# Performance work log

Hardware: AMD Instinct MI355X
Metric: run time of the kernel (lower is better)

## Reference

```python
import jax, jax.numpy as jnp
import numpy as np

B, S, E, H, L = 64, 256, 640, 512, 2  # batch, seq_len, input_size(=embed+sum_depth), rnn_size, num_layers
ZDIM = L * 2 * 2 * H  # ziphidden output dim = num_layers * num_dirs * (h|c) * H = 4096


def setup_inputs() -> dict:
    key = jax.random.key(0)
    ks = jax.random.split(key, 16)
    s = 0.05  # small init scale (~1/sqrt(H)) to avoid gate saturation
    f32 = jnp.float32
    inp = {
        "input": jax.random.normal(ks[0], (B, S, E), f32),
        "eps": jax.random.normal(ks[1], (B, ZDIM), f32),
        # layer 0 (input E), stacked over 2 directions [fwd, rev]
        "w_ih0": jax.random.normal(ks[2], (2, 4 * H, E), f32) * s,
        "w_hh0": jax.random.normal(ks[3], (2, 4 * H, H), f32) * s,
        "b_ih0": jax.random.normal(ks[4], (2, 4 * H), f32) * s,
        "b_hh0": jax.random.normal(ks[5], (2, 4 * H), f32) * s,
        # layer 1 (input 2H from bidirectional layer-0 output)
        "w_ih1": jax.random.normal(ks[6], (2, 4 * H, 2 * H), f32) * s,
        "w_hh1": jax.random.normal(ks[7], (2, 4 * H, H), f32) * s,
        "b_ih1": jax.random.normal(ks[8], (2, 4 * H), f32) * s,
        "b_hh1": jax.random.normal(ks[9], (2, 4 * H), f32) * s,
        # linear heads (layer_dim*2 -> layer_dim*2)
        "W_mu": jax.random.normal(ks[10], (ZDIM, ZDIM), f32) * 0.02,
        "b_mu": jax.random.normal(ks[11], (ZDIM,), f32) * 0.02,
        "W_var": jax.random.normal(ks[12], (ZDIM, ZDIM), f32) * 0.02,
        "b_var": jax.random.normal(ks[13], (ZDIM,), f32) * 0.02,
    }
    return inp


def _lstm_cell(x, h, c, wih, whh, b):
    # gates order i, f, g, o (PyTorch convention)
    g = x @ wih.T + h @ whh.T + b
    i, f, gg, o = jnp.split(g, 4, axis=-1)
    c2 = jax.nn.sigmoid(f) * c + jax.nn.sigmoid(i) * jnp.tanh(gg)
    h2 = jax.nn.sigmoid(o) * jnp.tanh(c2)
    return h2, c2


def reference(input, eps, w_ih0, w_hh0, b_ih0, b_hh0, w_ih1, w_hh1, b_ih1, b_hh1, W_mu, b_mu, W_var, b_var):
    # Module does input.view(seq_len, batch, embed) (a reshape, not transpose) then
    # steps the LSTM one timestep at a time for seq_len-1 steps. Since each call is
    # a length-1 sequence, both directions see the same single step independently.
    x_seq = input.reshape(S, B, E)[: S - 1]
    W_ih, W_hh = [w_ih0, w_ih1], [w_hh0, w_hh1]
    Bias = [b_ih0 + b_hh0, b_ih1 + b_hh1]

    h0 = jnp.zeros((2 * L, B, H), input.dtype)  # [l0f, l0r, l1f, l1r]
    c0 = jnp.zeros((2 * L, B, H), input.dtype)

    def step(carry, x):
        h, c = carry
        hs, cs = [], []
        inp_l = x
        for l in range(L):
            hf, cf = _lstm_cell(inp_l, h[2 * l], c[2 * l], W_ih[l][0], W_hh[l][0], Bias[l][0])
            hr, cr = _lstm_cell(inp_l, h[2 * l + 1], c[2 * l + 1], W_ih[l][1], W_hh[l][1], Bias[l][1])
            hs += [hf, hr]
            cs += [cf, cr]
            inp_l = jnp.concatenate([hf, hr], axis=-1)  # layer output feeds next layer
        return (jnp.stack(hs), jnp.stack(cs)), None

    (hF, cF), _ = jax.lax.scan(step, (h0, c0), x_seq)

    # ziphidden: cat(h, c, dim=2) -> transpose(0,1) -> view(B, -1)
    z = jnp.concatenate([hF, cF], axis=2)            # [2L, B, 2H]
    z = jnp.transpose(z, (1, 0, 2)).reshape(B, -1)   # [B, ZDIM]

    mu = z @ W_mu.T + b_mu
    logvar = z @ W_var.T + b_var
    # reparameterize (training mode) with externally supplied eps
    return mu + eps * jnp.exp(0.5 * logvar)
```

## Files before the change

kernel.cpp:

```cpp
#include <hip/hip_runtime.h>
#include <hip/hip_bf16.h>
#include <cstddef>
#include <cstdint>

#define B     64
#define S     256
#define E     640
#define H     512
#define TSTEPS (S - 1)
#define ZDIM  4096
#define KT    64
#define HS    (B * H)
#define CELL64 8192

typedef __attribute__((ext_vector_type(8)))  __bf16 bf16x8;
typedef __attribute__((ext_vector_type(16))) float  f32x16;
typedef unsigned long long ull;

__device__ __forceinline__ float sigf(float x) { return 1.0f / (1.0f + __expf(-x)); }
__device__ __forceinline__ float tanhfast(float x) { return 1.0f - 2.0f / (__expf(2.0f * x) + 1.0f); }

__device__ __forceinline__ unsigned short f2bf(float f) {
    union { float f; unsigned u; } x; x.f = f;
    unsigned r = x.u + 0x7fffu + ((x.u >> 16) & 1u);
    return (unsigned short)(r >> 16);
}
__device__ __forceinline__ float bf2f(unsigned short u) {
    union { unsigned u; float f; } x; x.u = ((unsigned)u) << 16;
    return x.f;
}
__device__ __forceinline__ unsigned pk2(float a, float b) {
    return (unsigned)f2bf(a) | ((unsigned)f2bf(b) << 16);
}

#define HSTORE64(p, v) __hip_atomic_store((p), (v), __ATOMIC_RELAXED, __HIP_MEMORY_SCOPE_AGENT)
#define HSTORE32(p, v) __hip_atomic_store((p), (v), __ATOMIC_RELAXED, __HIP_MEMORY_SCOPE_AGENT)
#define HLOAD32(p)     __hip_atomic_load((p), __ATOMIC_RELAXED, __HIP_MEMORY_SCOPE_AGENT)

__device__ __forceinline__ uint4 cld16(const void* p) {
    uint4 v;
    asm volatile("global_load_dwordx4 %0, %1, off sc0 sc1"
                 : "=v"(v) : "v"(p) : "memory");
    return v;
}
__device__ __forceinline__ void cwait0() {
    asm volatile("s_waitcnt vmcnt(0)" ::: "memory");
    __builtin_amdgcn_sched_barrier(0);
}
__device__ __forceinline__ bf16x8 u2b(uint4 u) {
    union { uint4 u; bf16x8 b; } x; x.u = u; return x.b;
}


__global__ __launch_bounds__(256) void conv_x_kernel(
    const float* __restrict__ in, unsigned short* __restrict__ out, int n8)
{
    int i = blockIdx.x * 256 + threadIdx.x;
    if (i >= n8) return;
    const float4* p = (const float4*)(in + (size_t)i * 8);
    float4 a = p[0], b = p[1];
    unsigned short* o = out + (size_t)i * 8;
    o[0] = f2bf(a.x); o[1] = f2bf(a.y); o[2] = f2bf(a.z); o[3] = f2bf(a.w);
    o[4] = f2bf(b.x); o[5] = f2bf(b.y); o[6] = f2bf(b.z); o[7] = f2bf(b.w);
}

__global__ __launch_bounds__(256) void repack_w_kernel(
    const float* __restrict__ in, unsigned short* __restrict__ out, int K)
{
    int kc = K / 8;
    int i = blockIdx.x * 256 + threadIdx.x;
    if (i >= 2 * 2048 * kc) return;
    int k8 = i % kc;
    int n  = (i / kc) & 2047;
    int d  = i / (kc * 2048);
    int srow = (n & 3) * 512 + (n >> 2);
    const float* src = in + ((size_t)d * 2048 + srow) * K + (size_t)k8 * 8;
    unsigned short* dst = out + ((size_t)d * 2048 + n) * K + (size_t)k8 * 8;
    #pragma unroll
    for (int q = 0; q < 8; ++q) dst[q] = f2bf(src[q]);
}

__global__ __launch_bounds__(256) void pack_bias_kernel(
    const float* __restrict__ bih, const float* __restrict__ bhh, float* __restrict__ out)
{
    int i = blockIdx.x * 256 + threadIdx.x;
    if (i >= 4096) return;
    int d = i >> 11, n = i & 2047;
    int s = d * 2048 + (n & 3) * 512 + (n >> 2);
    out[i] = bih[s] + bhh[s];
}

__global__ __launch_bounds__(256) void xproj_kernel(
    const unsigned short* __restrict__ xb,
    const unsigned short* __restrict__ w0p,
    unsigned short* __restrict__ xp)
{
    extern __shared__ __align__(16) char lds[];
    const int tid = threadIdx.x;
    const int l   = tid & 63;
    const int w   = tid >> 6;
    const int wm  = w & 1, wn = w >> 1;
    const int d   = blockIdx.x >> 5;
    const int n0  = (blockIdx.x & 31) * 64;

    for (int idx = tid; idx < 64 * 80; idx += 256) {
        int r = idx / 80, k8 = idx % 80;
        bf16x8 v = *(const bf16x8*)(w0p + ((size_t)d*2048 + n0 + r)*640 + (size_t)k8*8);
        int o = k8*16 + r*16; o -= (o >= 1280) ? 1280 : 0;
        *(bf16x8*)(lds + r*1280 + o) = v;
    }
    __syncthreads();

    const int lrow  = wn * 32 + (l & 31);
    const int khalf = l >> 5;
    const char* ldsrow = lds + (size_t)lrow * 1280;
    const int rot = lrow * 16 + khalf * 16;
    const int t0 = blockIdx.y * 64;
    const int t1 = (t0 + 64 < TSTEPS) ? (t0 + 64) : TSTEPS;

    for (int t = t0; t < t1; ++t) {
        f32x16 a0, a1;
#pragma unroll
        for (int r = 0; r < 16; ++r) { a0[r] = 0.f; a1[r] = 0.f; }
        const unsigned short* Ax = xb + ((size_t)t*B + wm*32 + (l & 31))*E + khalf*8;
#pragma unroll 8
        for (int k0 = 0; k0 < E; k0 += 16) {
            bf16x8 a = *(const bf16x8*)(Ax + k0);
            int o = k0*2 + rot; o -= (o >= 1280) ? 1280 : 0;
            bf16x8 b = *(const bf16x8*)(ldsrow + o);
            if ((k0 >> 4) & 1) a1 = __builtin_amdgcn_mfma_f32_32x32x16_bf16(a, b, a1, 0, 0, 0);
            else               a0 = __builtin_amdgcn_mfma_f32_32x32x16_bf16(a, b, a0, 0, 0, 0);
        }
        size_t base = ((((size_t)t*2 + d)*64 + (n0 >> 5) + wn)*2 + wm)*1024 + (size_t)l*16;
        unsigned short* dst = xp + base;
        uint4 o0, o1;
        o0.x = pk2(a0[0]+a1[0],  a0[1]+a1[1]);
        o0.y = pk2(a0[2]+a1[2],  a0[3]+a1[3]);
        o0.z = pk2(a0[4]+a1[4],  a0[5]+a1[5]);
        o0.w = pk2(a0[6]+a1[6],  a0[7]+a1[7]);
        o1.x = pk2(a0[8]+a1[8],  a0[9]+a1[9]);
        o1.y = pk2(a0[10]+a1[10], a0[11]+a1[11]);
        o1.z = pk2(a0[12]+a1[12], a0[13]+a1[13]);
        o1.w = pk2(a0[14]+a1[14], a0[15]+a1[15]);
        *(uint4*)dst       = o0;
        *(uint4*)(dst + 8) = o1;
    }
}

__device__ __forceinline__ void poll1(const unsigned* flags, int cell,
                                      unsigned tgt, int l)
{
    const unsigned* p0 = flags + (size_t)(cell*128 + l) * 16;
    for (;;) {
        unsigned a = HLOAD32(p0);
        unsigned b = HLOAD32(p0 + 64*16);
        unsigned v = a < b ? a : b;
        if (__all((int)(v >= tgt))) break;
        __builtin_amdgcn_s_sleep(1);
    }
}
__device__ __forceinline__ void poll2c(const unsigned* flags, int ca, int cb,
                                       unsigned tgt, int l)
{
    const unsigned* p0 = flags + (size_t)(ca*128 + l) * 16;
    const unsigned* p1 = flags + (size_t)(cb*128 + l) * 16;
    for (;;) {
        unsigned a = HLOAD32(p0);
        unsigned b = HLOAD32(p0 + 64*16);
        unsigned c = HLOAD32(p1);
        unsigned e = HLOAD32(p1 + 64*16);
        unsigned v = a < b ? a : b;
        unsigned u = c < e ? c : e;
        v = v < u ? v : u;
        if (__all((int)(v >= tgt))) break;
        __builtin_amdgcn_s_sleep(1);
    }
}

__device__ __forceinline__ void hcell_c_lds(const void* hp, const char* ldsrow,
    int rotofs, int wrapB, f32x16& a0, f32x16& a1)
{
    uint4 hv[32];
#pragma unroll
    for (int m = 0; m < 32; ++m)
        hv[m] = cld16((const char*)hp + (size_t)m * 1024);
    cwait0();
#pragma unroll
    for (int m = 0; m < 32; ++m) {
        int o = m*32 + rotofs; o -= (o >= wrapB) ? wrapB : 0;
        bf16x8 b = *(const bf16x8*)(ldsrow + o);
        bf16x8 a = u2b(hv[m]);
        if (m & 1) a1 = __builtin_amdgcn_mfma_f32_32x32x16_bf16(a, b, a1, 0, 0, 0);
        else       a0 = __builtin_amdgcn_mfma_f32_32x32x16_bf16(a, b, a0, 0, 0, 0);
    }
}

__device__ __forceinline__ void hcell_c_reg(const void* hp, const bf16x8* wh,
    f32x16& a0, f32x16& a1)
{
    uint4 hv[32];
#pragma unroll
    for (int m = 0; m < 32; ++m)
        hv[m] = cld16((const char*)hp + (size_t)m * 1024);
    cwait0();
#pragma unroll
    for (int m = 0; m < 32; ++m) {
        bf16x8 a = u2b(hv[m]);
        if (m & 1) a1 = __builtin_amdgcn_mfma_f32_32x32x16_bf16(a, wh[m], a1, 0, 0, 0);
        else       a0 = __builtin_amdgcn_mfma_f32_32x32x16_bf16(a, wh[m], a0, 0, 0, 0);
    }
}

template<bool XADD>
__device__ __forceinline__ void act_store(
    const f32x16& a0, const f32x16& a1, bf16x8 xpa, bf16x8 xpb,
    int unitg, int wm, int l, float* creg, float* hreg, ull* hq_cell)
{
    const int g  = l & 3;
    const int hi = l >> 5;
    union { bf16x8 v; unsigned short s[8]; } ua, ub;
    ua.v = xpa; ub.v = xpb;
    float gi[4], gf[4], gg[4], go[4];
#pragma unroll
    for (int r = 0; r < 16; ++r) {
        float v0 = a0[r] + a1[r];
        if (XADD) v0 += bf2f((r < 8) ? ua.s[r] : ub.s[r - 8]);
        float v1 = __shfl_xor(v0, 1);
        float v2 = __shfl_xor(v0, 2);
        float v3 = __shfl_xor(v0, 3);
        float pv[4] = {v0, v1, v2, v3};
        const int rg = r & 3, q = r >> 2;
        if (g == rg) { gi[q] = pv[rg^0]; gf[q] = pv[rg^1]; gg[q] = pv[rg^2]; go[q] = pv[rg^3]; }
    }
    const int ubase = unitg & ~3;
    ull* dst = hq_cell + wm*4096 + (ubase >> 4)*128 + ((ubase >> 3) & 1)*64
                       + ((ubase >> 2) & 1);
#pragma unroll
    for (int q = 0; q < 4; ++q) {
        int rl = g + 8*q + 4*hi;
        float cold = creg[q];
        float cnew = sigf(gf[q]) * cold + sigf(gi[q]) * tanhfast(gg[q]);
        float hnew = sigf(go[q]) * tanhfast(cnew);
        creg[q] = cnew;
        hreg[q] = hnew;
        unsigned m  = f2bf(hnew);
        unsigned o1 = __shfl_xor(m, 4);
        unsigned d0 = (unitg & 1) ? ((m << 16) | o1) : ((o1 << 16) | m);
        unsigned o2 = __shfl_xor(d0, 8);
        ull q64 = (unitg & 2) ? (((ull)d0 << 32) | (ull)o2) : (((ull)o2 << 32) | (ull)d0);
        if ((l & 12) == 0)
            HSTORE64(dst + rl*2, q64);
    }
}

template<int XPRE>
__global__ __launch_bounds__(256, 1) void persist_kernel(
    const unsigned short* __restrict__ xb,
    const unsigned short* __restrict__ w0p,
    const unsigned short* __restrict__ wh0p,
    const unsigned short* __restrict__ w1p,
    const unsigned short* __restrict__ wh1p,
    const float* __restrict__ b0p,
    const float* __restrict__ b1p,
    const unsigned short* __restrict__ xp,
    unsigned short* __restrict__ hbuf,
    float* __restrict__ cbuf,
    unsigned short* __restrict__ hplain,
    unsigned* __restrict__ flags)
{
    extern __shared__ __align__(16) char lds[];
    const int tid = threadIdx.x;
    const int l   = tid & 63;
    const int w   = tid >> 6;
    const int wm  = w & 1, wn = w >> 1;
    const int bid = blockIdx.x;
    const bool isL1 = bid >= 64;
    const int g2 = bid & 63;
    const int d  = g2 >> 5;
    const int n0 = (g2 & 31) * 64;
    const int myslot = g2 & 31;
    const int lrow  = wn * 32 + (l & 31);
    const int khalf = l >> 5;
    const int HHOFF = 64 * 1280;

    if (!isL1) {
        if (!XPRE) {
            for (int idx = tid; idx < 64 * 80; idx += 256) {
                int r = idx / 80, k8 = idx % 80;
                bf16x8 v = *(const bf16x8*)(w0p + ((size_t)d*2048 + n0 + r)*640 + (size_t)k8*8);
                int o = k8*16 + r*16; o -= (o >= 1280) ? 1280 : 0;
                *(bf16x8*)(lds + r*1280 + o) = v;
            }
        }
        const int hb0 = XPRE ? 0 : HHOFF;
        for (int idx = tid; idx < 64 * 64; idx += 256) {
            int r = idx / 64, k8 = idx % 64;
            bf16x8 v = *(const bf16x8*)(wh0p + ((size_t)d*2048 + n0 + r)*512 + (size_t)k8*8);
            int o = k8*16 + r*16; o -= (o >= 1024) ? 1024 : 0;
            *(bf16x8*)(lds + hb0 + r*1024 + o) = v;
        }
    } else {
        for (int idx = tid; idx < 64 * 128; idx += 256) {
            int r = idx / 128, k8 = idx % 128;
            bf16x8 v = *(const bf16x8*)(w1p + ((size_t)d*2048 + n0 + r)*1024 + (size_t)k8*8);
            int o = k8*16 + r*16; o -= (o >= 2048) ? 2048 : 0;
            *(bf16x8*)(lds + r*2048 + o) = v;
        }
    }
    __syncthreads();

    const float bias = (isL1 ? b1p : b0p)[d*2048 + n0 + lrow];
    const char* ldsrow_ih = lds + (size_t)lrow * (isL1 ? 2048 : 1280);
    const char* ldsrow_hh = lds + (XPRE ? 0 : HHOFF) + (size_t)lrow * 1024;
    const int rot = lrow * 16 + khalf * 16;
    const int unitg = ((n0 + lrow) >> 2);
    const int hoff  = wm*4096 + khalf*64 + (l & 31)*2;
    const int arow  = wm * 32 + (l & 31);
    float creg[4] = {0.f, 0.f, 0.f, 0.f};
    float hreg[4] = {0.f, 0.f, 0.f, 0.f};
    const ull* hb = (const ull*)hbuf;
    ull*       hw = (ull*)hbuf;
    const int mycell = isL1 ? (2 + d) : d;
    unsigned* myflag = flags + (size_t)(mycell*128 + myslot*4 + w) * 16;
    bf16x8 zero8 = {};

    bf16x8 wh[32];
    if (isL1) {
        const unsigned short* whl = wh1p + ((size_t)d*2048 + n0 + lrow)*512 + khalf*8;
#pragma unroll
        for (int m = 0; m < 32; ++m) wh[m] = *(const bf16x8*)(whl + m*16);
    }

    for (int k = 0; k <= TSTEPS; ++k) {
        const int rbuf = k % 3, wbuf = (k + 1) % 3;
        const size_t rb = (size_t)rbuf * 4 * CELL64;
        if (!isL1) {
            if (k < TSTEPS) {
                f32x16 a0, a1;
#pragma unroll
                for (int r = 0; r < 16; ++r) { a0[r] = bias; a1[r] = 0.f; }
                bf16x8 xpa = zero8, xpb = zero8;
                if (XPRE) {
                    size_t base = ((((size_t)k*2 + d)*64 + (n0 >> 5) + wn)*2 + wm)*1024
                                  + (size_t)l*16;
                    xpa = *(const bf16x8*)(xp + base);
                    xpb = *(const bf16x8*)(xp + base + 8);
                } else {
                    const unsigned short* Ax = xb + (size_t)k*B*E + (size_t)arow*E + khalf*8;
#pragma unroll 8
                    for (int k0 = 0; k0 < E; k0 += 16) {
                        bf16x8 a = *(const bf16x8*)(Ax + k0);
                        int o = k0*2 + rot; o -= (o >= 1280) ? 1280 : 0;
                        bf16x8 b = *(const bf16x8*)(ldsrow_ih + o);
                        if ((k0 >> 4) & 1) a1 = __builtin_amdgcn_mfma_f32_32x32x16_bf16(a, b, a1, 0, 0, 0);
                        else               a0 = __builtin_amdgcn_mfma_f32_32x32x16_bf16(a, b, a0, 0, 0, 0);
                    }
                }
                if (k >= 1) poll1(flags, d, (unsigned)k, l);
                hcell_c_lds((const char*)(hb + rb + (size_t)d*CELL64 + hoff),
                            ldsrow_hh, rot, 1024, a0, a1);
                if (k >= 3) poll2c(flags, 2, 3, (unsigned)(k - 2), l);
                act_store<true>(a0, a1, xpa, xpb, unitg, wm, l, creg, hreg,
                                hw + (size_t)wbuf*4*CELL64 + (size_t)d*CELL64);
                asm volatile("s_waitcnt vmcnt(0)" ::: "memory");
                if (l == 0) HSTORE32(myflag, (unsigned)(k + 1));
            }
        } else {
            if (k >= 1) {
                f32x16 a0, a1;
#pragma unroll
                for (int r = 0; r < 16; ++r) { a0[r] = bias; a1[r] = 0.f; }
                if (k >= 2) poll1(flags, 2 + d, (unsigned)(k - 1), l);
                hcell_c_reg((const char*)(hb + rb + (size_t)(2+d)*CELL64 + hoff),
                            wh, a0, a1);
                poll2c(flags, 0, 1, (unsigned)k, l);
                hcell_c_lds((const char*)(hb + rb + (size_t)0*CELL64 + hoff),
                            ldsrow_ih, rot, 2048, a0, a1);
                hcell_c_lds((const char*)(hb + rb + (size_t)1*CELL64 + hoff),
                            ldsrow_ih, rot + 1024, 2048, a0, a1);
                act_store<false>(a0, a1, zero8, zero8, unitg, wm, l, creg, hreg,
                                 hw + (size_t)wbuf*4*CELL64 + (size_t)(2+d)*CELL64);
                asm volatile("s_waitcnt vmcnt(0)" ::: "memory");
                if (l == 0) HSTORE32(myflag, (unsigned)k);
            }
        }
    }

    {
        float*          cc = cbuf   + (size_t)mycell * HS;
        unsigned short* hh = hplain + (size_t)mycell * HS;
        const int g = l & 3, hi = l >> 5;
#pragma unroll
        for (int q = 0; q < 4; ++q) {
            int row = 32*wm + g + 8*q + 4*hi;
            cc[(size_t)row * 512 + unitg] = creg[q];
            hh[(size_t)row * 512 + unitg] = f2bf(hreg[q]);
        }
    }
}

__global__ __launch_bounds__(256) void head_kernel(
    const unsigned short* __restrict__ hplain,
    const float* __restrict__ cbuf,
    const float* __restrict__ eps,
    const float* __restrict__ Wmu,  const float* __restrict__ bmu,
    const float* __restrict__ Wvar, const float* __restrict__ bvar,
    float* __restrict__ out)
{
    const int tid = threadIdx.x;
    const int b   = tid & 63;
    const int i   = blockIdx.x * 4 + (tid >> 6);

    __shared__ float zs[KT][B + 1];

    float amu = 0.f, alv = 0.f;
    const float* wm = Wmu  + (size_t)i * ZDIM;
    const float* wv = Wvar + (size_t)i * ZDIM;

    for (int k0 = 0; k0 < ZDIM; k0 += KT) {
        __syncthreads();
        for (int idx = tid; idx < (B * KT) / 4; idx += 256) {
            int bb  = idx / (KT / 4);
            int kq4 = (idx % (KT / 4)) * 4;
            int zk  = k0 + kq4;
            int cell = zk >> 10;
            int m    = zk & 1023;
            float4 v;
            if (m < H) {
                const unsigned short* hs = hplain + (size_t)cell * HS + (size_t)bb * H + m;
                v.x = bf2f(hs[0]); v.y = bf2f(hs[1]); v.z = bf2f(hs[2]); v.w = bf2f(hs[3]);
            } else {
                v = *(const float4*)(cbuf + (size_t)cell * HS + (size_t)bb * H + (m - H));
            }
            zs[kq4 + 0][bb] = v.x; zs[kq4 + 1][bb] = v.y;
            zs[kq4 + 2][bb] = v.z; zs[kq4 + 3][bb] = v.w;
        }
        __syncthreads();
        #pragma unroll
        for (int kk = 0; kk < KT; kk += 4) {
            float4 a = *(const float4*)(wm + k0 + kk);
            float4 c = *(const float4*)(wv + k0 + kk);
            float z0 = zs[kk + 0][b], z1 = zs[kk + 1][b];
            float z2 = zs[kk + 2][b], z3 = zs[kk + 3][b];
            amu += a.x * z0 + a.y * z1 + a.z * z2 + a.w * z3;
            alv += c.x * z0 + c.y * z1 + c.z * z2 + c.w * z3;
        }
    }
    float mu = amu + bmu[i];
    float lv = alv + bvar[i];
    out[(size_t)b * ZDIM + i] = mu + eps[(size_t)b * ZDIM + i] * __expf(0.5f * lv);
}

extern "C" void kernel_launch(void* const* d_in, const int* in_sizes, int n_in,
                              void* d_out, int out_size, void* d_ws, size_t ws_size,
                              hipStream_t stream) {
    const float* input = (const float*)d_in[0];
    const float* eps   = (const float*)d_in[1];
    const float* w_ih0 = (const float*)d_in[2];
    const float* w_hh0 = (const float*)d_in[3];
    const float* b_ih0 = (const float*)d_in[4];
    const float* b_hh0 = (const float*)d_in[5];
    const float* w_ih1 = (const float*)d_in[6];
    const float* w_hh1 = (const float*)d_in[7];
    const float* b_ih1 = (const float*)d_in[8];
    const float* b_hh1 = (const float*)d_in[9];
    const float* W_mu  = (const float*)d_in[10];
    const float* b_mu  = (const float*)d_in[11];
    const float* W_var = (const float*)d_in[12];
    const float* b_var = (const float*)d_in[13];
    float* out = (float*)d_out;

    uint8_t* base = (uint8_t*)d_ws;
    size_t off = 0;
    auto alloc = [&](size_t bytes) -> void* {
        void* p = base + off;
        off += (bytes + 255) & ~(size_t)255;
        return p;
    };
    unsigned short* xb   = (unsigned short*)alloc((size_t)TSTEPS * B * E * 2);
    unsigned short* w0p  = (unsigned short*)alloc((size_t)2 * 2048 * E * 2);
    unsigned short* wh0p = (unsigned short*)alloc((size_t)2 * 2048 * H * 2);
    unsigned short* w1p  = (unsigned short*)alloc((size_t)2 * 2048 * 1024 * 2);
    unsigned short* wh1p = (unsigned short*)alloc((size_t)2 * 2048 * H * 2);
    float* b0p = (float*)alloc(2 * 2048 * 4);
    float* b1p = (float*)alloc(2 * 2048 * 4);
    unsigned* flags      = (unsigned*)alloc(4 * 128 * 64);
    unsigned short* hbuf = (unsigned short*)alloc((size_t)3 * 4 * HS * 2);
    float* cbuf          = (float*)alloc((size_t)4 * HS * 4);
    unsigned short* hplain = (unsigned short*)alloc((size_t)4 * HS * 2);
    size_t off_noxp = off;
    unsigned short* xp   = (unsigned short*)alloc((size_t)TSTEPS * 2 * 2048 * B * 2);
    const bool XPRE = (ws_size >= off);
    (void)off_noxp;

    hipMemsetAsync(flags, 0, 4 * 128 * 64 + (size_t)3 * 4 * HS * 2, stream);

    conv_x_kernel<<<(TSTEPS * B * E / 8 + 255) / 256, 256, 0, stream>>>(input, xb, TSTEPS * B * E / 8);
    repack_w_kernel<<<(2 * 2048 * (E / 8) + 255) / 256, 256, 0, stream>>>(w_ih0, w0p, E);
    repack_w_kernel<<<(2 * 2048 * (H / 8) + 255) / 256, 256, 0, stream>>>(w_hh0, wh0p, H);
    repack_w_kernel<<<(2 * 2048 * (1024 / 8) + 255) / 256, 256, 0, stream>>>(w_ih1, w1p, 1024);
    repack_w_kernel<<<(2 * 2048 * (H / 8) + 255) / 256, 256, 0, stream>>>(w_hh1, wh1p, H);
    pack_bias_kernel<<<16, 256, 0, stream>>>(b_ih0, b_hh0, b0p);
    pack_bias_kernel<<<16, 256, 0, stream>>>(b_ih1, b_hh1, b1p);

    const size_t lds_persist = 144 * 1024;
    if (XPRE) {
        const size_t lds_xp = 84 * 1024;
        hipFuncSetAttribute((const void*)xproj_kernel,
                            hipFuncAttributeMaxDynamicSharedMemorySize, (int)lds_xp);
        xproj_kernel<<<dim3(64, 4), 256, lds_xp, stream>>>(xb, w0p, xp);
        hipFuncSetAttribute((const void*)persist_kernel<1>,
                            hipFuncAttributeMaxDynamicSharedMemorySize, (int)lds_persist);
        persist_kernel<1><<<128, 256, lds_persist, stream>>>(
            xb, w0p, wh0p, w1p, wh1p, b0p, b1p, xp, hbuf, cbuf, hplain, flags);
    } else {
        hipFuncSetAttribute((const void*)persist_kernel<0>,
                            hipFuncAttributeMaxDynamicSharedMemorySize, (int)lds_persist);
        persist_kernel<0><<<128, 256, lds_persist, stream>>>(
            xb, w0p, wh0p, w1p, wh1p, b0p, b1p, xp, hbuf, cbuf, hplain, flags);
    }

    head_kernel<<<ZDIM / 4, 256, 0, stream>>>(hplain, cbuf, eps, W_mu, b_mu, W_var, b_var, out);
}
```

Measured before the change: 3.298 ms.

## Use four h buffers and merge layer-0 RAW/WAR flag polls into one loop

Extends the rotating hidden-state buffer from three to four slots, which relaxes the write-after-read constraint so layer 0 only needs layer 1 to reach step k-3. The RAW poll on its own direction and the WAR poll on the layer-1 cells are combined into a single polling loop before the recurrent matmul, removing one polling phase from the per-step critical path. Flag loads now use inline-asm cache-bypassing global loads issued together with one waitcnt. The cost is one more h buffer of workspace and memset, and the code relies on the asm loads being coherent.

```diff
diff --git a/kernel.cpp b/kernel.cpp
--- a/kernel.cpp
+++ b/kernel.cpp
@@ -12,6 +12,7 @@
 #define KT    64
 #define HS    (B * H)
 #define CELL64 8192
+#define NBUF  4
 
 typedef __attribute__((ext_vector_type(8)))  __bf16 bf16x8;
 typedef __attribute__((ext_vector_type(16))) float  f32x16;
@@ -35,11 +36,16 @@
 
 #define HSTORE64(p, v) __hip_atomic_store((p), (v), __ATOMIC_RELAXED, __HIP_MEMORY_SCOPE_AGENT)
 #define HSTORE32(p, v) __hip_atomic_store((p), (v), __ATOMIC_RELAXED, __HIP_MEMORY_SCOPE_AGENT)
-#define HLOAD32(p)     __hip_atomic_load((p), __ATOMIC_RELAXED, __HIP_MEMORY_SCOPE_AGENT)
 
 __device__ __forceinline__ uint4 cld16(const void* p) {
     uint4 v;
     asm volatile("global_load_dwordx4 %0, %1, off sc0 sc1"
+                 : "=v"(v) : "v"(p) : "memory");
+    return v;
+}
+__device__ __forceinline__ unsigned ldf(const unsigned* p) {
+    unsigned v;
+    asm volatile("global_load_dword %0, %1, off sc0 sc1"
                  : "=v"(v) : "v"(p) : "memory");
     return v;
 }
@@ -147,30 +153,48 @@
     }
 }
 
-__device__ __forceinline__ void poll1(const unsigned* flags, int cell,
-                                      unsigned tgt, int l)
+__device__ __forceinline__ void poll_l0(const unsigned* flags, int d,
+                                        unsigned traw, unsigned twar, int l)
+{
+    const unsigned* pd = flags + (size_t)(d*128 + l) * 16;
+    const unsigned* p2 = flags + (size_t)(2*128 + l) * 16;
+    const unsigned* p3 = flags + (size_t)(3*128 + l) * 16;
+    for (;;) {
+        unsigned a0 = ldf(pd), a1 = ldf(pd + 64*16);
+        unsigned b0 = ldf(p2), b1 = ldf(p2 + 64*16);
+        unsigned c0 = ldf(p3), c1 = ldf(p3 + 64*16);
+        cwait0();
+        unsigned ra = a0 < a1 ? a0 : a1;
+        unsigned wb = b0 < b1 ? b0 : b1;
+        unsigned wc = c0 < c1 ? c0 : c1;
+        unsigned ww = wb < wc ? wb : wc;
+        if (__all((int)(ra >= traw && ww >= twar))) break;
+        __builtin_amdgcn_s_sleep(1);
+    }
+}
+__device__ __forceinline__ void poll_1c(const unsigned* flags, int cell,
+                                        unsigned tgt, int l)
 {
     const unsigned* p0 = flags + (size_t)(cell*128 + l) * 16;
     for (;;) {
-        unsigned a = HLOAD32(p0);
-        unsigned b = HLOAD32(p0 + 64*16);
-        unsigned v = a < b ? a : b;
+        unsigned a0 = ldf(p0), a1 = ldf(p0 + 64*16);
+        cwait0();
+        unsigned v = a0 < a1 ? a0 : a1;
         if (__all((int)(v >= tgt))) break;
         __builtin_amdgcn_s_sleep(1);
     }
 }
-__device__ __forceinline__ void poll2c(const unsigned* flags, int ca, int cb,
-                                       unsigned tgt, int l)
+__device__ __forceinline__ void poll_2c(const unsigned* flags, int ca, int cb,
+                                        unsigned tgt, int l)
 {
     const unsigned* p0 = flags + (size_t)(ca*128 + l) * 16;
     const unsigned* p1 = flags + (size_t)(cb*128 + l) * 16;
     for (;;) {
-        unsigned a = HLOAD32(p0);
-        unsigned b = HLOAD32(p0 + 64*16);
-        unsigned c = HLOAD32(p1);
-        unsigned e = HLOAD32(p1 + 64*16);
-        unsigned v = a < b ? a : b;
-        unsigned u = c < e ? c : e;
+        unsigned a0 = ldf(p0), a1 = ldf(p0 + 64*16);
+        unsigned b0 = ldf(p1), b1 = ldf(p1 + 64*16);
+        cwait0();
+        unsigned v = a0 < a1 ? a0 : a1;
+        unsigned u = b0 < b1 ? b0 : b1;
         v = v < u ? v : u;
         if (__all((int)(v >= tgt))) break;
         __builtin_amdgcn_s_sleep(1);
@@ -332,8 +356,9 @@
     }
 
     for (int k = 0; k <= TSTEPS; ++k) {
-        const int rbuf = k % 3, wbuf = (k + 1) % 3;
+        const int rbuf = k % NBUF, wbuf = (k + 1) % NBUF;
         const size_t rb = (size_t)rbuf * 4 * CELL64;
+        const size_t wb = (size_t)wbuf * 4 * CELL64;
         if (!isL1) {
             if (k < TSTEPS) {
                 f32x16 a0, a1;
@@ -356,12 +381,13 @@
                         else               a0 = __builtin_amdgcn_mfma_f32_32x32x16_bf16(a, b, a0, 0, 0, 0);
                     }
                 }
-                if (k >= 1) poll1(flags, d, (unsigned)k, l);
+                if (k >= 1)
+                    poll_l0(flags, d, (unsigned)k,
+                            (k >= 3) ? (unsigned)(k - 3) : 0u, l);
                 hcell_c_lds((const char*)(hb + rb + (size_t)d*CELL64 + hoff),
                             ldsrow_hh, rot, 1024, a0, a1);
-                if (k >= 3) poll2c(flags, 2, 3, (unsigned)(k - 2), l);
                 act_store<true>(a0, a1, xpa, xpb, unitg, wm, l, creg, hreg,
-                                hw + (size_t)wbuf*4*CELL64 + (size_t)d*CELL64);
+                                hw + wb + (size_t)d*CELL64);
                 asm volatile("s_waitcnt vmcnt(0)" ::: "memory");
                 if (l == 0) HSTORE32(myflag, (unsigned)(k + 1));
             }
@@ -370,16 +396,16 @@
                 f32x16 a0, a1;
 #pragma unroll
                 for (int r = 0; r < 16; ++r) { a0[r] = bias; a1[r] = 0.f; }
-                if (k >= 2) poll1(flags, 2 + d, (unsigned)(k - 1), l);
+                if (k >= 2) poll_1c(flags, 2 + d, (unsigned)(k - 1), l);
                 hcell_c_reg((const char*)(hb + rb + (size_t)(2+d)*CELL64 + hoff),
                             wh, a0, a1);
-                poll2c(flags, 0, 1, (unsigned)k, l);
+                poll_2c(flags, 0, 1, (unsigned)k, l);
                 hcell_c_lds((const char*)(hb + rb + (size_t)0*CELL64 + hoff),
                             ldsrow_ih, rot, 2048, a0, a1);
                 hcell_c_lds((const char*)(hb + rb + (size_t)1*CELL64 + hoff),
                             ldsrow_ih, rot + 1024, 2048, a0, a1);
                 act_store<false>(a0, a1, zero8, zero8, unitg, wm, l, creg, hreg,
-                                 hw + (size_t)wbuf*4*CELL64 + (size_t)(2+d)*CELL64);
+                                 hw + wb + (size_t)(2+d)*CELL64);
                 asm volatile("s_waitcnt vmcnt(0)" ::: "memory");
                 if (l == 0) HSTORE32(myflag, (unsigned)k);
             }
@@ -485,15 +511,13 @@
     float* b0p = (float*)alloc(2 * 2048 * 4);
     float* b1p = (float*)alloc(2 * 2048 * 4);
     unsigned* flags      = (unsigned*)alloc(4 * 128 * 64);
-    unsigned short* hbuf = (unsigned short*)alloc((size_t)3 * 4 * HS * 2);
+    unsigned short* hbuf = (unsigned short*)alloc((size_t)NBUF * 4 * HS * 2);
     float* cbuf          = (float*)alloc((size_t)4 * HS * 4);
     unsigned short* hplain = (unsigned short*)alloc((size_t)4 * HS * 2);
-    size_t off_noxp = off;
     unsigned short* xp   = (unsigned short*)alloc((size_t)TSTEPS * 2 * 2048 * B * 2);
     const bool XPRE = (ws_size >= off);
-    (void)off_noxp;
-
-    hipMemsetAsync(flags, 0, 4 * 128 * 64 + (size_t)3 * 4 * HS * 2, stream);
+
+    hipMemsetAsync(flags, 0, 4 * 128 * 64 + (size_t)NBUF * 4 * HS * 2, stream);
 
     conv_x_kernel<<<(TSTEPS * B * E / 8 + 255) / 256, 256, 0, stream>>>(input, xb, TSTEPS * B * E / 8);
     repack_w_kernel<<<(2 * 2048 * (E / 8) + 255) / 256, 256, 0, stream>>>(w_ih0, w0p, E);
```

After: 3.245 ms. About the same (-1.6%).
